# Kernel tuning notes

Measured on AMD Instinct MI355X. Metric: run time of the kernel, lower is better.

## Reference

```python
import jax, jax.numpy as jnp
import numpy as np
from jax import lax

N_STEPS = 4  # matches init n_steps


def setup_inputs() -> dict:
    key = jax.random.key(0)
    ks = jax.random.split(key, 12)
    B, N, D, E = 32, 256, 512, 4
    prop_state = jax.random.normal(ks[0], (B, N, D), dtype=jnp.float32)
    edges = (jax.random.uniform(ks[1], (B, N, N * E * 2)) < 0.02).astype(jnp.float32)
    s = 0.02  # matches weight.data.normal_(0.0, 0.02)
    return {
        "prop_state": prop_state,
        "edges": edges,
        "W_in": jax.random.normal(ks[2], (E, D, D), dtype=jnp.float32) * s,
        "b_in": jnp.zeros((E, D), jnp.float32),
        "W_out": jax.random.normal(ks[3], (E, D, D), dtype=jnp.float32) * s,
        "b_out": jnp.zeros((E, D), jnp.float32),
        "W_r": jax.random.normal(ks[4], (3 * D, D), dtype=jnp.float32) * s,
        "b_r": jnp.zeros((D,), jnp.float32),
        "W_z": jax.random.normal(ks[5], (3 * D, D), dtype=jnp.float32) * s,
        "b_z": jnp.zeros((D,), jnp.float32),
        "W_h": jax.random.normal(ks[6], (3 * D, D), dtype=jnp.float32) * s,
        "b_h": jnp.zeros((D,), jnp.float32),
        "W_bridge_h": jax.random.normal(ks[7], (D, D), dtype=jnp.float32) * s,
        "b_bridge_h": jnp.zeros((D,), jnp.float32),
        "W_bridge_c": jax.random.normal(ks[8], (D, D), dtype=jnp.float32) * s,
        "b_bridge_c": jnp.zeros((D,), jnp.float32),
    }


def reference(prop_state, edges, W_in, b_in, W_out, b_out,
              W_r, b_r, W_z, b_z, W_h, b_h,
              W_bridge_h, b_bridge_h, W_bridge_c, b_bridge_c):
    B, N, D = prop_state.shape
    E = W_in.shape[0]
    edges_in = edges[:, :, : N * E]   # [B, N, N*E]
    edges_out = edges[:, :, N * E:]   # [B, N, N*E]

    def step(state, _):
        # per-edge-type linear transforms, edge-type-major layout [B, E*N, D]
        ins = (jnp.einsum('bnd,edh->bend', state, W_in)
               + b_in[None, :, None, :]).reshape(B, E * N, D)
        outs = (jnp.einsum('bnd,edh->bend', state, W_out)
                + b_out[None, :, None, :]).reshape(B, E * N, D)
        a_in = jnp.einsum('bnm,bmd->bnd', edges_in, ins)    # bmm aggregation
        a_out = jnp.einsum('bnm,bmd->bnd', edges_out, outs)
        a = jnp.concatenate([a_in, a_out, state], axis=2)   # [B, N, 3D]
        r = jax.nn.sigmoid(a @ W_r + b_r)
        z = jax.nn.sigmoid(a @ W_z + b_z)
        joined = jnp.concatenate([a_in, a_out, r * state], axis=2)
        h_hat = jax.nn.leaky_relu(joined @ W_h + b_h)        # slope 0.01 as torch
        return (1.0 - z) * state + z * h_hat, None

    state, _ = lax.scan(step, prop_state, None, length=N_STEPS)

    # bridge (bridge_extra_node=False path): mean over dim 0, 4 stacked copies
    join = state.mean(axis=0)                     # [N, D]
    js = jnp.broadcast_to(join, (4,) + join.shape)  # [4, N, D]
    h = jax.nn.relu(js @ W_bridge_h + b_bridge_h)
    c = jax.nn.relu(js @ W_bridge_c + b_bridge_c)
    return state, h, c
```

## Files before the change

kernel.cpp:

```cpp
#include <hip/hip_runtime.h>
#include <math.h>


typedef __bf16 bf16_t;
typedef __bf16 bf16x8 __attribute__((ext_vector_type(8)));
typedef __bf16 bf16x4_t __attribute__((ext_vector_type(4)));
typedef float f32x4 __attribute__((ext_vector_type(4)));

__device__ __forceinline__ void stage_lds16(const bf16_t* __restrict__ g, int ld,
                                            bf16_t* __restrict__ s) {
  int wave = threadIdx.x >> 6;
  int lane = threadIdx.x & 63;
  int rsub = lane >> 2;
  int k0 = (lane & 3) << 3;
#pragma unroll
  for (int i = 0; i < 2; ++i) {
    int c = wave + (i << 2);
    const bf16_t* gp = g + (size_t)((c << 4) + rsub) * ld + k0;
    __builtin_amdgcn_global_load_lds(
        (const __attribute__((address_space(1))) void*)gp,
        (__attribute__((address_space(3))) void*)(s + (c << 9)), 16, 0, 0);
  }
}

__device__ __forceinline__ void stage_lds16_64(const bf16_t* __restrict__ g, int ld,
                                               bf16_t* __restrict__ s) {
  int wave = threadIdx.x >> 6;
  int lane = threadIdx.x & 63;
  int rsub = lane >> 2;
  int k0 = (lane & 3) << 3;
  const bf16_t* gp = g + (size_t)((wave << 4) + rsub) * ld + k0;
  __builtin_amdgcn_global_load_lds(
      (const __attribute__((address_space(1))) void*)gp,
      (__attribute__((address_space(3))) void*)(s + (wave << 9)), 16, 0, 0);
}

__device__ __forceinline__ bf16x8 frag(const bf16_t* s, int r, int koff) {
  return *reinterpret_cast<const bf16x8*>(s + (r << 5) + koff);
}

#define SBAR() __builtin_amdgcn_s_barrier()
#define SCHED0() __builtin_amdgcn_sched_barrier(0)


__global__ __launch_bounds__(256) void k_build_idx(const float* __restrict__ edges,
                                                   unsigned short* __restrict__ nbr,
                                                   uchar4* __restrict__ cnt4) {
  int wid = threadIdx.x >> 6, lane = threadIdx.x & 63;
  int W = blockIdx.x * 4 + wid;
  int b = W >> 9, io = (W >> 8) & 1, n = W & 255;
  const float* p = edges + (size_t)(b * 256 + n) * 2048 + io * 1024;
  unsigned short* list = nbr + (size_t)W * 64;
  int base = 0;
  int ends[4];
#pragma unroll
  for (int e = 0; e < 4; ++e) {
#pragma unroll
    for (int ch = 0; ch < 4; ++ch) {
      int c = e * 256 + ch * 64 + lane;
      float v = p[c];
      unsigned long long mask = __ballot(v != 0.0f);
      int before = __popcll(mask & ((1ull << lane) - 1ull));
      if (v != 0.0f && (base + before) < 64) list[base + before] = (unsigned short)c;
      base += __popcll(mask);
    }
    ends[e] = base < 64 ? base : 64;
  }
  if (lane == 0)
    cnt4[W] = make_uchar4((unsigned char)ends[0], (unsigned char)ends[1],
                          (unsigned char)ends[2], (unsigned char)ends[3]);
}

__global__ __launch_bounds__(256) void k_rowsum(const float* __restrict__ W,
                                                float* __restrict__ wsum, int nrows) {
  int wid = threadIdx.x >> 6, lane = threadIdx.x & 63;
  int row = blockIdx.x * 4 + wid;
  if (row >= nrows) return;
  const float4* p = reinterpret_cast<const float4*>(W + (size_t)row * 512);
  float s = 0.f;
#pragma unroll
  for (int i = 0; i < 2; ++i) {
    float4 v = p[lane + i * 64];
    s += v.x + v.y + v.z + v.w;
  }
#pragma unroll
  for (int off = 32; off > 0; off >>= 1) s += __shfl_down(s, off, 64);
  if (lane == 0) wsum[row] = s;
}

__global__ __launch_bounds__(256) void k_prep_wall(const float* __restrict__ Wr,
                                                   const float* __restrict__ Wz,
                                                   const float* __restrict__ Wh,
                                                   bf16_t* __restrict__ dst) {
  __shared__ float tile[32][33];
  int z = blockIdx.z;
  const float* src = z == 0 ? Wr : z == 1 ? Wz : Wh;
  int Ksrc = z == 2 ? 1024 : 1536;
  bf16_t* d = dst + (size_t)(z * 512) * 1536;
  int tx = threadIdx.x & 31, ty = threadIdx.x >> 5;
  int n0 = blockIdx.x * 32, k0 = blockIdx.y * 32;
  if (k0 >= Ksrc) {
#pragma unroll
    for (int i = 0; i < 4; ++i)
      d[(size_t)(n0 + ty + i * 8) * 1536 + k0 + tx] = (bf16_t)0.0f;
    return;
  }
#pragma unroll
  for (int i = 0; i < 4; ++i)
    tile[ty + i * 8][tx] = src[(size_t)(k0 + ty + i * 8) * 512 + n0 + tx];
  __syncthreads();
#pragma unroll
  for (int i = 0; i < 4; ++i)
    d[(size_t)(n0 + ty + i * 8) * 1536 + k0 + tx] = (bf16_t)tile[tx][ty + i * 8];
}

__global__ __launch_bounds__(256) void k_prep_small(const float* __restrict__ Whb_src,
                                                    const float* __restrict__ Wbh_src,
                                                    const float* __restrict__ Wbc_src,
                                                    bf16_t* __restrict__ Whb_t,
                                                    bf16_t* __restrict__ Wbh_t,
                                                    bf16_t* __restrict__ Wbc_t) {
  __shared__ float tile[32][33];
  int z = blockIdx.z;
  const float* src = z == 0 ? Whb_src : z == 1 ? Wbh_src : Wbc_src;
  bf16_t* dst = z == 0 ? Whb_t : z == 1 ? Wbh_t : Wbc_t;
  int tx = threadIdx.x & 31, ty = threadIdx.x >> 5;
  int n0 = blockIdx.x * 32, k0 = blockIdx.y * 32;
#pragma unroll
  for (int i = 0; i < 4; ++i)
    tile[ty + i * 8][tx] = src[(size_t)(k0 + ty + i * 8) * 512 + n0 + tx];
  __syncthreads();
#pragma unroll
  for (int i = 0; i < 4; ++i)
    dst[(size_t)(n0 + ty + i * 8) * 512 + k0 + tx] = (bf16_t)tile[tx][ty + i * 8];
}

__global__ __launch_bounds__(256) void k_state_init(const float* __restrict__ src,
                                                    float* __restrict__ dst_f32,
                                                    bf16_t* __restrict__ dst_b, int n4) {
  int i = blockIdx.x * 256 + threadIdx.x;
  if (i < n4) {
    float4 v = reinterpret_cast<const float4*>(src)[i];
    reinterpret_cast<float4*>(dst_f32)[i] = v;
    bf16x4_t o;
    o[0] = (bf16_t)v.x; o[1] = (bf16_t)v.y; o[2] = (bf16_t)v.z; o[3] = (bf16_t)v.w;
    *reinterpret_cast<bf16x4_t*>(dst_b + i * 4) = o;
  }
}

__global__ __launch_bounds__(256) void k_agg_sparse(const unsigned short* __restrict__ nbr,
                                                    const uchar4* __restrict__ cnt4,
                                                    const bf16_t* __restrict__ state_b,
                                                    const float* __restrict__ wsum_in,
                                                    const float* __restrict__ wsum_out,
                                                    const float* __restrict__ b_in,
                                                    const float* __restrict__ b_out,
                                                    bf16_t* __restrict__ ain_b,
                                                    bf16_t* __restrict__ aout_b) {
  int wid = threadIdx.x >> 6, lane = threadIdx.x & 63;
  int W = blockIdx.x * 4 + wid;
  int b = W >> 9, io = (W >> 8) & 1, n = W & 255;
  const float* wsel = io ? wsum_out : wsum_in;
  const float* bsel = io ? b_out : b_in;
  int d0 = lane << 3;
  float w[4][8], bi[4][8];
#pragma unroll
  for (int e = 0; e < 4; ++e) {
#pragma unroll
    for (int t = 0; t < 8; t += 4) {
      float4 v = *reinterpret_cast<const float4*>(wsel + e * 512 + d0 + t);
      w[e][t] = v.x; w[e][t + 1] = v.y; w[e][t + 2] = v.z; w[e][t + 3] = v.w;
      float4 u = *reinterpret_cast<const float4*>(bsel + e * 512 + d0 + t);
      bi[e][t] = u.x; bi[e][t + 1] = u.y; bi[e][t + 2] = u.z; bi[e][t + 3] = u.w;
    }
  }
  int mycode = nbr[(size_t)W * 64 + lane];
  uchar4 ce = cnt4[W];
  float acc[8];
#pragma unroll
  for (int t = 0; t < 8; ++t) acc[t] = 0.f;
  const bf16_t* Sb = state_b + ((size_t)b << 17) + d0;
  int start = 0;
#pragma unroll
  for (int e = 0; e < 4; ++e) {
    int end = (e == 0) ? ce.x : (e == 1) ? ce.y : (e == 2) ? ce.z : ce.w;
    float fc = (float)(end - start);
#pragma unroll
    for (int t = 0; t < 8; ++t) acc[t] += fc * bi[e][t];
    for (int j = start; j < end; ++j) {
      int c = __shfl(mycode, j, 64);
      int m = c & 255;
      bf16x8 s = *reinterpret_cast<const bf16x8*>(Sb + ((size_t)m << 9));
#pragma unroll
      for (int t = 0; t < 8; ++t) acc[t] += (float)s[t] * w[e][t];
    }
    start = end;
  }
  bf16x8 o;
#pragma unroll
  for (int t = 0; t < 8; ++t) o[t] = (bf16_t)acc[t];
  bf16_t* dst = io ? aout_b : ain_b;
  *reinterpret_cast<bf16x8*>(dst + (size_t)(b * 256 + n) * 512 + d0) = o;
}

__global__ __launch_bounds__(256, 4) void k_gates(const bf16_t* __restrict__ ain_b,
                                                  const bf16_t* __restrict__ aout_b,
                                                  const bf16_t* __restrict__ state_row_b,
                                                  const bf16_t* __restrict__ Wall_t,
                                                  const float* __restrict__ b_r,
                                                  const float* __restrict__ b_z,
                                                  const float* __restrict__ b_h,
                                                  bf16_t* __restrict__ rs_b,
                                                  bf16_t* __restrict__ zb_b,
                                                  bf16_t* __restrict__ hp_b) {
  __shared__ __align__(16) char smem[32768];
  float* tr = (float*)smem;
  int mt = blockIdx.x, nt = blockIdx.y;
  int gm0 = mt * 128, gn0 = nt * 128;
  int lane = threadIdx.x & 63, wid = threadIdx.x >> 6;
  int wr = wid >> 1, wc = wid & 1;
  int l15 = lane & 15, q = lane >> 4, koff = q << 3;
  int nkt = (nt < 8) ? 48 : 32;
  f32x4 acc[4][4];
#pragma unroll
  for (int i = 0; i < 4; ++i)
#pragma unroll
    for (int j = 0; j < 4; ++j) acc[i][j] = f32x4{0.f, 0.f, 0.f, 0.f};

  auto stageAB = [&](int buf, int kt) {
    int blk = kt >> 4, kk = (kt & 15) << 5;
    const bf16_t* gA = (blk == 0 ? ain_b : blk == 1 ? aout_b : state_row_b)
                       + (size_t)gm0 * 512 + kk;
    bf16_t* base = (bf16_t*)(smem + buf * 16384);
    stage_lds16(gA, 512, base);
    stage_lds16(Wall_t + (size_t)gn0 * 1536 + (kt << 5), 1536, base + 4096);
  };

  stageAB(0, 0);
  stageAB(1, 1);
  for (int kt = 0; kt < nkt; ++kt) {
    if (kt + 1 < nkt)
      asm volatile("s_waitcnt vmcnt(4)" ::: "memory");
    else
      asm volatile("s_waitcnt vmcnt(0)" ::: "memory");
    SCHED0(); SBAR(); SCHED0();
    const bf16_t* As = (const bf16_t*)(smem + (kt & 1) * 16384);
    const bf16_t* Bs = As + 4096;
    bf16x8 af[4], bfr[4];
#pragma unroll
    for (int i = 0; i < 4; ++i) af[i] = frag(As, wr * 64 + i * 16 + l15, koff);
#pragma unroll
    for (int j = 0; j < 4; ++j) bfr[j] = frag(Bs, wc * 64 + j * 16 + l15, koff);
#pragma unroll
    for (int i = 0; i < 4; ++i)
#pragma unroll
      for (int j = 0; j < 4; ++j)
        acc[i][j] = __builtin_amdgcn_mfma_f32_16x16x32_bf16(af[i], bfr[j], acc[i][j], 0, 0, 0);
    SCHED0(); SBAR(); SCHED0();
    if (kt + 2 < nkt) stageAB(kt & 1, kt + 2);
  }

  int region = nt >> 2;
  int cn0 = gn0 - region * 512;
  const float* bias = region == 0 ? b_r : region == 1 ? b_z : b_h;
#pragma unroll
  for (int p = 0; p < 4; ++p) {
    __syncthreads();
    if (wc == (p >> 1)) {
      int j0 = (p & 1) << 1;
#pragma unroll
      for (int jj = 0; jj < 2; ++jj) {
        int j = j0 + jj;
        int c = j * 16 + l15 - ((p & 1) << 5);
#pragma unroll
        for (int i = 0; i < 4; ++i)
#pragma unroll
          for (int rr = 0; rr < 4; ++rr) {
            int row = wr * 64 + i * 16 + q * 4 + rr;
            tr[row * 36 + c] = acc[i][j][rr];
          }
      }
    }
    __syncthreads();
#pragma unroll
    for (int s = 0; s < 16; ++s) {
      int e = threadIdx.x + (s << 8);
      int row = e >> 5, c = e & 31;
      int col = cn0 + (p << 5) + c;
      size_t idx = (size_t)(gm0 + row) * 512 + col;
      float x = tr[row * 36 + c] + bias[col];
      if (region == 0) {
        float rg = 1.0f / (1.0f + __expf(-x));
        rs_b[idx] = (bf16_t)(rg * (float)state_row_b[idx]);
      } else if (region == 1) {
        zb_b[idx] = (bf16_t)(1.0f / (1.0f + __expf(-x)));
      } else {
        hp_b[idx] = (bf16_t)x;
      }
    }
  }
}

__global__ __launch_bounds__(256, 4) void k_gru(const bf16_t* __restrict__ rs_b,
                                                const bf16_t* __restrict__ Whb_t,
                                                const bf16_t* __restrict__ hp_b,
                                                const bf16_t* __restrict__ zb_b,
                                                float* __restrict__ state_f32,
                                                bf16_t* __restrict__ state_row_b) {
  __shared__ __align__(16) char smem[24576];
  float* tr = (float*)smem;
  int mt = blockIdx.x, nt = blockIdx.y;
  int gm0 = mt * 64, gn0 = nt * 128;
  int lane = threadIdx.x & 63, wid = threadIdx.x >> 6;
  int wr = wid >> 1, wc = wid & 1;
  int l15 = lane & 15, q = lane >> 4, koff = q << 3;
  f32x4 acc[2][4];
#pragma unroll
  for (int i = 0; i < 2; ++i)
#pragma unroll
    for (int j = 0; j < 4; ++j) acc[i][j] = f32x4{0.f, 0.f, 0.f, 0.f};

  auto stageAB = [&](int buf, int kt) {
    bf16_t* base = (bf16_t*)(smem + buf * 12288);
    stage_lds16_64(rs_b + (size_t)gm0 * 512 + (kt << 5), 512, base);
    stage_lds16(Whb_t + (size_t)gn0 * 512 + (kt << 5), 512, base + 2048);
  };

  stageAB(0, 0);
  stageAB(1, 1);
  for (int kt = 0; kt < 16; ++kt) {
    if (kt + 1 < 16)
      asm volatile("s_waitcnt vmcnt(3)" ::: "memory");
    else
      asm volatile("s_waitcnt vmcnt(0)" ::: "memory");
    SCHED0(); SBAR(); SCHED0();
    const bf16_t* As = (const bf16_t*)(smem + (kt & 1) * 12288);
    const bf16_t* Bs = As + 2048;
    bf16x8 af[2], bfr[4];
#pragma unroll
    for (int i = 0; i < 2; ++i) af[i] = frag(As, wr * 32 + i * 16 + l15, koff);
#pragma unroll
    for (int j = 0; j < 4; ++j) bfr[j] = frag(Bs, wc * 64 + j * 16 + l15, koff);
#pragma unroll
    for (int i = 0; i < 2; ++i)
#pragma unroll
      for (int j = 0; j < 4; ++j)
        acc[i][j] = __builtin_amdgcn_mfma_f32_16x16x32_bf16(af[i], bfr[j], acc[i][j], 0, 0, 0);
    SCHED0(); SBAR(); SCHED0();
    if (kt + 2 < 16) stageAB(kt & 1, kt + 2);
  }

#pragma unroll
  for (int p = 0; p < 4; ++p) {
    __syncthreads();
    if (wc == (p >> 1)) {
      int j0 = (p & 1) << 1;
#pragma unroll
      for (int jj = 0; jj < 2; ++jj) {
        int j = j0 + jj;
        int c = j * 16 + l15 - ((p & 1) << 5);
#pragma unroll
        for (int i = 0; i < 2; ++i)
#pragma unroll
          for (int rr = 0; rr < 4; ++rr) {
            int row = wr * 32 + i * 16 + q * 4 + rr;
            tr[row * 36 + c] = acc[i][j][rr];
          }
      }
    }
    __syncthreads();
#pragma unroll
    for (int s = 0; s < 8; ++s) {
      int e = threadIdx.x + (s << 8);
      int row = e >> 5, c = e & 31;
      int col = gn0 + (p << 5) + c;
      size_t idx = (size_t)(gm0 + row) * 512 + col;
      float x = tr[row * 36 + c] + (float)hp_b[idx];
      float hh = x > 0.0f ? x : 0.01f * x;
      float z = (float)zb_b[idx];
      float so = state_f32[idx];
      float sn = (1.0f - z) * so + z * hh;
      state_f32[idx] = sn;
      state_row_b[idx] = (bf16_t)sn;
    }
  }
}


__global__ __launch_bounds__(256) void k_join(const float* __restrict__ state_f32,
                                              bf16_t* __restrict__ join_b) {
  int idx = blockIdx.x * 256 + threadIdx.x;
  float s = 0.f;
#pragma unroll
  for (int b = 0; b < 32; ++b) s += state_f32[(size_t)b * 131072 + idx];
  join_b[idx] = (bf16_t)(s * (1.0f / 32.0f));
}

__global__ __launch_bounds__(256) void k_bridge(const bf16_t* __restrict__ join_b,
                                                const bf16_t* __restrict__ Wbh_t,
                                                const bf16_t* __restrict__ Wbc_t,
                                                const float* __restrict__ b_bh,
                                                const float* __restrict__ b_bc,
                                                float* __restrict__ out_h,
                                                float* __restrict__ out_c) {
  __shared__ bf16_t As[2][4096];
  __shared__ bf16_t Bs[2][4096];
  int mt = blockIdx.x, nt = blockIdx.y, hc = blockIdx.z;
  const bf16_t* Wt = hc ? Wbc_t : Wbh_t;
  const float* bias = hc ? b_bc : b_bh;
  float* dst = hc ? out_c : out_h;
  int gm0 = mt * 128, gn0 = nt * 128;
  int lane = threadIdx.x & 63, wid = threadIdx.x >> 6;
  int wr = wid >> 1, wc = wid & 1;
  int l15 = lane & 15, koff = (lane >> 4) << 3;
  f32x4 acc[4][4];
#pragma unroll
  for (int i = 0; i < 4; ++i)
#pragma unroll
    for (int j = 0; j < 4; ++j) acc[i][j] = f32x4{0.f, 0.f, 0.f, 0.f};
  auto stageAB = [&](int buf, int kt) {
    stage_lds16(join_b + (size_t)gm0 * 512 + (kt << 5), 512, As[buf]);
    stage_lds16(Wt + (size_t)gn0 * 512 + (kt << 5), 512, Bs[buf]);
  };
  stageAB(0, 0);
  __syncthreads();
  int cur = 0;
  for (int kt = 0; kt < 16; ++kt) {
    if (kt + 1 < 16) stageAB(cur ^ 1, kt + 1);
    bf16x8 af[4], bfr[4];
#pragma unroll
    for (int i = 0; i < 4; ++i) af[i] = frag(As[cur], wr * 64 + i * 16 + l15, koff);
#pragma unroll
    for (int j = 0; j < 4; ++j) bfr[j] = frag(Bs[cur], wc * 64 + j * 16 + l15, koff);
#pragma unroll
    for (int i = 0; i < 4; ++i)
#pragma unroll
      for (int j = 0; j < 4; ++j)
        acc[i][j] = __builtin_amdgcn_mfma_f32_16x16x32_bf16(af[i], bfr[j], acc[i][j], 0, 0, 0);
    __syncthreads();
    cur ^= 1;
  }
  int lr0 = (lane >> 4) << 2;
#pragma unroll
  for (int j = 0; j < 4; ++j) {
    int col = gn0 + wc * 64 + j * 16 + l15;
    float bv = bias[col];
#pragma unroll
    for (int i = 0; i < 4; ++i) {
#pragma unroll
      for (int r = 0; r < 4; ++r) {
        int row = gm0 + wr * 64 + i * 16 + lr0 + r;
        float v = acc[i][j][r] + bv;
        v = v > 0.f ? v : 0.f;
#pragma unroll
        for (int rep = 0; rep < 4; ++rep)
          dst[(size_t)rep * 131072 + (size_t)row * 512 + col] = v;
      }
    }
  }
}


extern "C" void kernel_launch(void* const* d_in, const int* in_sizes, int n_in,
                              void* d_out, int out_size, void* d_ws, size_t ws_size,
                              hipStream_t stream) {
  const float* prop_state = (const float*)d_in[0];
  const float* edges = (const float*)d_in[1];
  const float* W_in = (const float*)d_in[2];
  const float* b_in = (const float*)d_in[3];
  const float* W_out = (const float*)d_in[4];
  const float* b_out = (const float*)d_in[5];
  const float* W_r = (const float*)d_in[6];
  const float* b_r = (const float*)d_in[7];
  const float* W_z = (const float*)d_in[8];
  const float* b_z = (const float*)d_in[9];
  const float* W_h = (const float*)d_in[10];
  const float* b_h = (const float*)d_in[11];
  const float* W_bh = (const float*)d_in[12];
  const float* b_bh = (const float*)d_in[13];
  const float* W_bc = (const float*)d_in[14];
  const float* b_bc = (const float*)d_in[15];

  float* out_state = (float*)d_out;
  float* out_h = out_state + 4194304;
  float* out_c = out_h + 524288;

  char* ws = (char*)d_ws;
  size_t off = 0;
  auto alloc = [&](size_t bytes) -> void* {
    void* p = ws + off;
    off += (bytes + 255) & ~(size_t)255;
    return p;
  };
  unsigned short* nbr = (unsigned short*)alloc(16384ull * 64 * 2);
  uchar4* cnt4   = (uchar4*)alloc(16384ull * 4);
  float* wsum_in  = (float*)alloc(2048ull * 4);
  float* wsum_out = (float*)alloc(2048ull * 4);
  bf16_t* Wall_t = (bf16_t*)alloc(1536ull * 1536 * 2);
  bf16_t* Whb_t  = (bf16_t*)alloc(512ull * 512 * 2);
  bf16_t* Wbh_t  = (bf16_t*)alloc(512ull * 512 * 2);
  bf16_t* Wbc_t  = (bf16_t*)alloc(512ull * 512 * 2);
  bf16_t* state_b = (bf16_t*)alloc(4194304ull * 2);
  bf16_t* ain_b  = (bf16_t*)alloc(4194304ull * 2);
  bf16_t* aout_b = (bf16_t*)alloc(4194304ull * 2);
  bf16_t* rs_b   = (bf16_t*)alloc(4194304ull * 2);
  bf16_t* zb_b   = (bf16_t*)alloc(4194304ull * 2);
  bf16_t* hp_b   = (bf16_t*)alloc(4194304ull * 2);
  bf16_t* join_b = (bf16_t*)alloc(131072ull * 2);
  if (off > ws_size) return;

  k_build_idx<<<4096, 256, 0, stream>>>(edges, nbr, cnt4);
  k_rowsum<<<512, 256, 0, stream>>>(W_in, wsum_in, 2048);
  k_rowsum<<<512, 256, 0, stream>>>(W_out, wsum_out, 2048);
  k_prep_wall<<<dim3(16, 48, 3), 256, 0, stream>>>(W_r, W_z, W_h, Wall_t);
  k_prep_small<<<dim3(16, 16, 3), 256, 0, stream>>>(W_h + 1024 * 512, W_bh, W_bc,
                                                    Whb_t, Wbh_t, Wbc_t);
  k_state_init<<<4096, 256, 0, stream>>>(prop_state, out_state, state_b, 1048576);

  for (int step = 0; step < 4; ++step) {
    k_agg_sparse<<<4096, 256, 0, stream>>>(nbr, cnt4, state_b, wsum_in, wsum_out,
                                           b_in, b_out, ain_b, aout_b);
    k_gates<<<dim3(64, 12), 256, 0, stream>>>(ain_b, aout_b, state_b, Wall_t,
                                              b_r, b_z, b_h, rs_b, zb_b, hp_b);
    k_gru<<<dim3(128, 4), 256, 0, stream>>>(rs_b, Whb_t, hp_b, zb_b,
                                            out_state, state_b);
  }

  k_join<<<512, 256, 0, stream>>>(out_state, join_b);
  k_bridge<<<dim3(2, 4, 2), 256, 0, stream>>>(join_b, Wbh_t, Wbc_t, b_bh, b_bc, out_h, out_c);
}
```

Before: 544.3 us.

## Enlarge k_gates tile to 256x128 with 512 threads and simpler double buffering

The gates GEMM moves from 128x128 tiles with 256 threads to 256x128 tiles with 512 threads. Each wave now computes a 128x32 sub-tile, and the grid shrinks from 64x12 to 32x12 blocks. The pipeline changes from a two-ahead prefetch with explicit vmcnt waits to a single-ahead prefetch, issued before compute, with __syncthreads barriers. This should cut redundant weight loads, but it halves the block count to 384, which may underfill the CUs. It also relies on plain __syncthreads rather than explicit vmcnt waits to complete the async LDS loads before the next tile is read.

```diff
diff --git a/kernel.cpp b/kernel.cpp
--- a/kernel.cpp
+++ b/kernel.cpp
@@ -6,6 +6,9 @@
 typedef __bf16 bf16x8 __attribute__((ext_vector_type(8)));
 typedef __bf16 bf16x4_t __attribute__((ext_vector_type(4)));
 typedef float f32x4 __attribute__((ext_vector_type(4)));
+
+#define SBAR() __builtin_amdgcn_s_barrier()
+#define SCHED0() __builtin_amdgcn_sched_barrier(0)
 
 __device__ __forceinline__ void stage_lds16(const bf16_t* __restrict__ g, int ld,
                                             bf16_t* __restrict__ s) {
@@ -35,12 +38,37 @@
       (__attribute__((address_space(3))) void*)(s + (wave << 9)), 16, 0, 0);
 }
 
+__device__ __forceinline__ void stage_lds16_256_w8(const bf16_t* __restrict__ g, int ld,
+                                                   bf16_t* __restrict__ s) {
+  int wave = threadIdx.x >> 6;
+  int lane = threadIdx.x & 63;
+  int rsub = lane >> 2;
+  int k0 = (lane & 3) << 3;
+#pragma unroll
+  for (int i = 0; i < 2; ++i) {
+    int c = wave + (i << 3);
+    const bf16_t* gp = g + (size_t)((c << 4) + rsub) * ld + k0;
+    __builtin_amdgcn_global_load_lds(
+        (const __attribute__((address_space(1))) void*)gp,
+        (__attribute__((address_space(3))) void*)(s + (c << 9)), 16, 0, 0);
+  }
+}
+
+__device__ __forceinline__ void stage_lds16_128_w8(const bf16_t* __restrict__ g, int ld,
+                                                   bf16_t* __restrict__ s) {
+  int wave = threadIdx.x >> 6;
+  int lane = threadIdx.x & 63;
+  int rsub = lane >> 2;
+  int k0 = (lane & 3) << 3;
+  const bf16_t* gp = g + (size_t)((wave << 4) + rsub) * ld + k0;
+  __builtin_amdgcn_global_load_lds(
+      (const __attribute__((address_space(1))) void*)gp,
+      (__attribute__((address_space(3))) void*)(s + (wave << 9)), 16, 0, 0);
+}
+
 __device__ __forceinline__ bf16x8 frag(const bf16_t* s, int r, int koff) {
   return *reinterpret_cast<const bf16x8*>(s + (r << 5) + koff);
 }
-
-#define SBAR() __builtin_amdgcn_s_barrier()
-#define SCHED0() __builtin_amdgcn_sched_barrier(0)
 
 
 __global__ __launch_bounds__(256) void k_build_idx(const float* __restrict__ edges,
@@ -203,7 +231,7 @@
   *reinterpret_cast<bf16x8*>(dst + (size_t)(b * 256 + n) * 512 + d0) = o;
 }
 
-__global__ __launch_bounds__(256, 4) void k_gates(const bf16_t* __restrict__ ain_b,
+__global__ __launch_bounds__(512, 4) void k_gates(const bf16_t* __restrict__ ain_b,
                                                   const bf16_t* __restrict__ aout_b,
                                                   const bf16_t* __restrict__ state_row_b,
                                                   const bf16_t* __restrict__ Wall_t,
@@ -213,51 +241,50 @@
                                                   bf16_t* __restrict__ rs_b,
                                                   bf16_t* __restrict__ zb_b,
                                                   bf16_t* __restrict__ hp_b) {
-  __shared__ __align__(16) char smem[32768];
+  __shared__ __align__(16) char smem[49152];
   float* tr = (float*)smem;
+  int tid = threadIdx.x;
+  int lane = tid & 63, wid = tid >> 6;
+  int wr = wid >> 2, wc = wid & 3;
   int mt = blockIdx.x, nt = blockIdx.y;
-  int gm0 = mt * 128, gn0 = nt * 128;
-  int lane = threadIdx.x & 63, wid = threadIdx.x >> 6;
-  int wr = wid >> 1, wc = wid & 1;
+  int gm0 = mt * 256, gn0 = nt * 128;
   int l15 = lane & 15, q = lane >> 4, koff = q << 3;
   int nkt = (nt < 8) ? 48 : 32;
-  f32x4 acc[4][4];
-#pragma unroll
-  for (int i = 0; i < 4; ++i)
-#pragma unroll
-    for (int j = 0; j < 4; ++j) acc[i][j] = f32x4{0.f, 0.f, 0.f, 0.f};
+  f32x4 acc[8][2];
+#pragma unroll
+  for (int i = 0; i < 8; ++i)
+#pragma unroll
+    for (int j = 0; j < 2; ++j) acc[i][j] = f32x4{0.f, 0.f, 0.f, 0.f};
 
   auto stageAB = [&](int buf, int kt) {
     int blk = kt >> 4, kk = (kt & 15) << 5;
     const bf16_t* gA = (blk == 0 ? ain_b : blk == 1 ? aout_b : state_row_b)
                        + (size_t)gm0 * 512 + kk;
-    bf16_t* base = (bf16_t*)(smem + buf * 16384);
-    stage_lds16(gA, 512, base);
-    stage_lds16(Wall_t + (size_t)gn0 * 1536 + (kt << 5), 1536, base + 4096);
+    bf16_t* base = (bf16_t*)(smem + buf * 24576);
+    stage_lds16_256_w8(gA, 512, base);
+    stage_lds16_128_w8(Wall_t + (size_t)gn0 * 1536 + (kt << 5), 1536,
+                       base + 8192);
   };
 
   stageAB(0, 0);
-  stageAB(1, 1);
+  __syncthreads();
+  int cur = 0;
   for (int kt = 0; kt < nkt; ++kt) {
-    if (kt + 1 < nkt)
-      asm volatile("s_waitcnt vmcnt(4)" ::: "memory");
-    else
-      asm volatile("s_waitcnt vmcnt(0)" ::: "memory");
-    SCHED0(); SBAR(); SCHED0();
-    const bf16_t* As = (const bf16_t*)(smem + (kt & 1) * 16384);
-    const bf16_t* Bs = As + 4096;
-    bf16x8 af[4], bfr[4];
-#pragma unroll
-    for (int i = 0; i < 4; ++i) af[i] = frag(As, wr * 64 + i * 16 + l15, koff);
-#pragma unroll
-    for (int j = 0; j < 4; ++j) bfr[j] = frag(Bs, wc * 64 + j * 16 + l15, koff);
-#pragma unroll
-    for (int i = 0; i < 4; ++i)
-#pragma unroll
-      for (int j = 0; j < 4; ++j)
+    if (kt + 1 < nkt) stageAB(cur ^ 1, kt + 1);
+    const bf16_t* As = (const bf16_t*)(smem + cur * 24576);
+    const bf16_t* Bs = As + 8192;
+    bf16x8 af[8], bfr[2];
+#pragma unroll
+    for (int i = 0; i < 8; ++i) af[i] = frag(As, wr * 128 + i * 16 + l15, koff);
+#pragma unroll
+    for (int j = 0; j < 2; ++j) bfr[j] = frag(Bs, wc * 32 + j * 16 + l15, koff);
+#pragma unroll
+    for (int i = 0; i < 8; ++i)
+#pragma unroll
+      for (int j = 0; j < 2; ++j)
         acc[i][j] = __builtin_amdgcn_mfma_f32_16x16x32_bf16(af[i], bfr[j], acc[i][j], 0, 0, 0);
-    SCHED0(); SBAR(); SCHED0();
-    if (kt + 2 < nkt) stageAB(kt & 1, kt + 2);
+    __syncthreads();
+    cur ^= 1;
   }
 
   int region = nt >> 2;
@@ -266,25 +293,19 @@
 #pragma unroll
   for (int p = 0; p < 4; ++p) {
     __syncthreads();
-    if (wc == (p >> 1)) {
-      int j0 = (p & 1) << 1;
-#pragma unroll
-      for (int jj = 0; jj < 2; ++jj) {
-        int j = j0 + jj;
-        int c = j * 16 + l15 - ((p & 1) << 5);
-#pragma unroll
-        for (int i = 0; i < 4; ++i)
-#pragma unroll
-          for (int rr = 0; rr < 4; ++rr) {
-            int row = wr * 64 + i * 16 + q * 4 + rr;
-            tr[row * 36 + c] = acc[i][j][rr];
-          }
-      }
+    if (wc == p) {
+#pragma unroll
+      for (int i = 0; i < 8; ++i)
+#pragma unroll
+        for (int j = 0; j < 2; ++j)
+#pragma unroll
+          for (int rr = 0; rr < 4; ++rr)
+            tr[(wr * 128 + i * 16 + q * 4 + rr) * 36 + j * 16 + l15] = acc[i][j][rr];
     }
     __syncthreads();
 #pragma unroll
     for (int s = 0; s < 16; ++s) {
-      int e = threadIdx.x + (s << 8);
+      int e = tid + (s << 9);
       int row = e >> 5, c = e & 31;
       int col = cn0 + (p << 5) + c;
       size_t idx = (size_t)(gm0 + row) * 512 + col;
@@ -520,7 +541,7 @@
   for (int step = 0; step < 4; ++step) {
     k_agg_sparse<<<4096, 256, 0, stream>>>(nbr, cnt4, state_b, wsum_in, wsum_out,
                                            b_in, b_out, ain_b, aout_b);
-    k_gates<<<dim3(64, 12), 256, 0, stream>>>(ain_b, aout_b, state_b, Wall_t,
+    k_gates<<<dim3(32, 12), 512, 0, stream>>>(ain_b, aout_b, state_b, Wall_t,
                                               b_r, b_z, b_h, rs_b, zb_b, hp_b);
     k_gru<<<dim3(128, 4), 256, 0, stream>>>(rs_b, Whb_t, hp_b, zb_b,
                                             out_state, state_b);
```

New measurement: 559.4 us. 2.8% more time.
